# Performance work log

Hardware: AMD Instinct MI355X
Metric: run time of the kernel (lower is better)

## Reference

```python
import jax, jax.numpy as jnp
import numpy as np
import math

N = 100000   # nodes
E = 1600000  # edges (avg degree 16)
D = 128      # in_dim == out_dim
H = 8        # heads
DK = D // H  # 16


def setup_inputs() -> dict:
    key = jax.random.key(0)
    ks = jax.random.split(key, 16)
    s = 1.0 / math.sqrt(D)
    inp = {
        "h": jax.random.normal(ks[0], (N, D), dtype=jnp.float32),
        "src": jax.random.randint(ks[1], (E,), 0, N, dtype=jnp.int32),
        "dst": jax.random.randint(ks[2], (E,), 0, N, dtype=jnp.int32),
        # linear params (torch Linear: y = x @ W.T + b)
        "Wk": jax.random.normal(ks[3], (D, D), dtype=jnp.float32) * s,
        "bk": jnp.zeros((D,), dtype=jnp.float32),
        "Wq": jax.random.normal(ks[4], (D, D), dtype=jnp.float32) * s,
        "bq": jnp.zeros((D,), dtype=jnp.float32),
        "Wv": jax.random.normal(ks[5], (D, D), dtype=jnp.float32) * s,
        "bv": jnp.zeros((D,), dtype=jnp.float32),
        "Wa": jax.random.normal(ks[6], (D, D), dtype=jnp.float32) * s,
        "ba": jnp.zeros((D,), dtype=jnp.float32),
        # relation params
        "rel_att": jax.random.normal(ks[7], (H, DK, DK), dtype=jnp.float32) * (1.0 / math.sqrt(DK)),
        "rel_msg": jax.random.normal(ks[8], (H, DK, DK), dtype=jnp.float32) * (1.0 / math.sqrt(DK)),
        "rel_pri": jnp.ones((H,), dtype=jnp.float32),
        "skip": jnp.ones((1,), dtype=jnp.float32),
    }
    return inp


def reference(h, src, dst, Wk, bk, Wq, bq, Wv, bv, Wa, ba, rel_att, rel_msg, rel_pri, skip):
    sqrt_dk = math.sqrt(DK)
    # per-node projections -> [N, H, DK]
    k = (h @ Wk.T + bk).reshape(N, H, DK)
    q = (h @ Wq.T + bq).reshape(N, H, DK)
    v = (h @ Wv.T + bv).reshape(N, H, DK)
    # per-relation transforms on k and v
    k = jnp.einsum('nhd,hde->nhe', k, rel_att)
    v = jnp.einsum('nhd,hde->nhe', v, rel_msg)
    # edge scores: dot(q[dst], k[src]) per head -> [E, H]
    score = jnp.einsum('ehd,ehd->eh', q[dst], k[src])
    score = score * rel_pri / sqrt_dk
    # edge softmax normalized over incoming edges of each dst node
    smax = jax.ops.segment_max(score, dst, num_segments=N)        # [N, H]
    ex = jnp.exp(score - smax[dst])                               # [E, H]
    denom = jax.ops.segment_sum(ex, dst, num_segments=N)         # [N, H]
    attn = ex / denom[dst]                                       # [E, H]
    # weighted scatter-aggregation of source values
    msg = v[src] * attn[:, :, None]                               # [E, H, DK]
    t = jax.ops.segment_sum(msg, dst, num_segments=N)             # [N, H, DK]
    t = t.reshape(N, D)
    # target-specific aggregation with learned skip gate (dropout=0 eval, norm=Identity)
    trans_out = t @ Wa.T + ba
    alpha = jax.nn.sigmoid(skip[0])
    new_h = trans_out * alpha + h * (1.0 - alpha)
    return new_h
```

## Files before the change

### kernel.cpp

```cpp
#include <hip/hip_runtime.h>
#include <hip/hip_bf16.h>
#include <math.h>

#define NN 100000
#define EE 1600000
#define DD 128
#define HH 8
#define LDW 136
#define BSH 9
#define NB 196
#define EPB 8192
#define A_BLOCKS 196
#define GEMM_BLOCKS 782

typedef short short8 __attribute__((ext_vector_type(8)));
typedef float f32x4 __attribute__((ext_vector_type(4)));

__device__ __forceinline__ unsigned short f2bf(float f) {
    unsigned int u = __float_as_uint(f);
    u += 0x7fffu + ((u >> 16) & 1u);
    return (unsigned short)(u >> 16);
}
__device__ __forceinline__ float bf2f(unsigned short h) {
    return __uint_as_float((unsigned int)h << 16);
}
__device__ __forceinline__ void cvt8(const float4& a, const float4& b,
                                     short8& h8, short8& l8) {
    float vals[8] = {a.x, a.y, a.z, a.w, b.x, b.y, b.z, b.w};
    #pragma unroll
    for (int j = 0; j < 8; j++) {
        unsigned short hi = f2bf(vals[j]);
        h8[j] = (short)hi;
        l8[j] = (short)f2bf(vals[j] - bf2f(hi));
    }
}

__device__ __forceinline__ void prep_work(int which, int bx,
                             const float* __restrict__ Wq, const float* __restrict__ Wk,
                             const float* __restrict__ Wv, const float* __restrict__ Wa,
                             const float* __restrict__ bq, const float* __restrict__ bk,
                             const float* __restrict__ bv, const float* __restrict__ ba,
                             const float* __restrict__ rel_att, const float* __restrict__ rel_msg,
                             unsigned short* __restrict__ WH, unsigned short* __restrict__ WL,
                             float* __restrict__ BE) {
    int o = bx * 256 + threadIdx.x;
    int j = o >> 7, c = o & 127;
    float val;
    if (which == 0) {
        val = Wq[o];
        if (o < 128) BE[o] = bq[o];
    } else if (which == 3) {
        val = Wa[o];
        if (o < 128) BE[384 + o] = ba[o];
    } else {
        const float* rel = (which == 1) ? rel_att : rel_msg;
        const float* W   = (which == 1) ? Wk : Wv;
        const float* b   = (which == 1) ? bk : bv;
        int hh = j >> 4, e = j & 15;
        val = 0.f;
        #pragma unroll
        for (int d = 0; d < 16; d++)
            val += rel[hh * 256 + d * 16 + e] * W[(hh * 16 + d) * 128 + c];
        if (c == 0) {
            float bacc = 0.f;
            #pragma unroll
            for (int d = 0; d < 16; d++)
                bacc += b[hh * 16 + d] * rel[hh * 256 + d * 16 + e];
            BE[which * 128 + j] = bacc;
        }
    }
    unsigned short hi = f2bf(val);
    unsigned short lo = f2bf(val - bf2f(hi));
    WH[which * 16384 + o] = hi;
    WL[which * 16384 + o] = lo;
}

__global__ void prep_hist(const float* __restrict__ Wq, const float* __restrict__ Wk,
                          const float* __restrict__ Wv, const float* __restrict__ Wa,
                          const float* __restrict__ bq, const float* __restrict__ bk,
                          const float* __restrict__ bv, const float* __restrict__ ba,
                          const float* __restrict__ rel_att, const float* __restrict__ rel_msg,
                          unsigned short* __restrict__ WH, unsigned short* __restrict__ WL,
                          float* __restrict__ BE,
                          const int* __restrict__ dst, int* __restrict__ bcnt) {
    __shared__ int lh[NB];
    int bid = blockIdx.x;
    if (bid < 256) {
        prep_work(bid >> 6, bid & 63, Wq, Wk, Wv, Wa, bq, bk, bv, ba,
                  rel_att, rel_msg, WH, WL, BE);
    } else {
        int t = threadIdx.x;
        for (int i = t; i < NB; i += 256) lh[i] = 0;
        __syncthreads();
        int base = (bid - 256) * EPB;
        int cnt = min(EPB, EE - base);
        for (int i = t; i < cnt; i += 256)
            atomicAdd(&lh[dst[base + i] >> BSH], 1);
        __syncthreads();
        for (int i = t; i < NB; i += 256)
            if (lh[i]) atomicAdd(&bcnt[i], lh[i]);
    }
}

__device__ __forceinline__ void gemm_body(char* smemc, int base,
                         const float* __restrict__ x,
                         const unsigned short* __restrict__ WH,
                         const unsigned short* __restrict__ WL,
                         const float* __restrict__ BE, int nw,
                         float* __restrict__ out0, unsigned short* __restrict__ kvout,
                         const float* __restrict__ resid, const float* __restrict__ skip) {
    unsigned short* wh = (unsigned short*)smemc;
    unsigned short* wl = wh + 128 * LDW;
    int tid = threadIdx.x;
    int wv = tid >> 6, lane = tid & 63;
    int lrow = lane & 15, quad = lane >> 4;

    short8 ah[2][4], al[2][4];
    float4 fz = {0.f, 0.f, 0.f, 0.f};
    #pragma unroll
    for (int mt = 0; mt < 2; mt++) {
        int row = base + wv * 32 + mt * 16 + lrow;
        const float* xr = x + (size_t)row * 128;
        bool ok = (row < NN);
        #pragma unroll
        for (int kc = 0; kc < 4; kc++) {
            int off = kc * 32 + quad * 8;
            float4 a = ok ? *(const float4*)&xr[off] : fz;
            float4 b = ok ? *(const float4*)&xr[off + 4] : fz;
            cvt8(a, b, ah[mt][kc], al[mt][kc]);
        }
    }

    float alpha = 1.f, beta = 0.f;
    if (resid) {
        float sv = skip[0];
        alpha = 1.f / (1.f + expf(-sv));
        beta = 1.f - alpha;
    }

    for (int wi = 0; wi < nw; wi++) {
        __syncthreads();
        const unsigned short* WHp = WH + wi * 16384;
        const unsigned short* WLp = WL + wi * 16384;
        for (int i = tid; i < 128 * 16; i += 256) {
            int n = i >> 4, kq = (i & 15) << 3;
            *(uint4*)&wh[n * LDW + kq] = *(const uint4*)&WHp[n * 128 + kq];
            *(uint4*)&wl[n * LDW + kq] = *(const uint4*)&WLp[n * 128 + kq];
        }
        __syncthreads();

        f32x4 zero4 = {0.f, 0.f, 0.f, 0.f};
        f32x4 acc[2][8];
        #pragma unroll
        for (int a = 0; a < 2; a++)
            #pragma unroll
            for (int b = 0; b < 8; b++) acc[a][b] = zero4;

        #pragma unroll
        for (int kc = 0; kc < 4; kc++) {
            #pragma unroll
            for (int nt = 0; nt < 8; nt++) {
                int koff = kc * 32 + quad * 8;
                int brow = (nt * 16 + lrow) * LDW + koff;
                short8 bh = *(const short8*)&wh[brow];
                short8 bl = *(const short8*)&wl[brow];
                acc[0][nt] = __builtin_amdgcn_mfma_f32_16x16x32_bf16(ah[0][kc], bh, acc[0][nt], 0, 0, 0);
                acc[1][nt] = __builtin_amdgcn_mfma_f32_16x16x32_bf16(ah[1][kc], bh, acc[1][nt], 0, 0, 0);
                acc[0][nt] = __builtin_amdgcn_mfma_f32_16x16x32_bf16(al[0][kc], bh, acc[0][nt], 0, 0, 0);
                acc[1][nt] = __builtin_amdgcn_mfma_f32_16x16x32_bf16(al[1][kc], bh, acc[1][nt], 0, 0, 0);
                acc[0][nt] = __builtin_amdgcn_mfma_f32_16x16x32_bf16(ah[0][kc], bl, acc[0][nt], 0, 0, 0);
                acc[1][nt] = __builtin_amdgcn_mfma_f32_16x16x32_bf16(ah[1][kc], bl, acc[1][nt], 0, 0, 0);
            }
        }

        const float* be = BE + wi * 128;
        #pragma unroll
        for (int nt = 0; nt < 8; nt++) {
            int col = nt * 16 + lrow;
            float bb = be[col];
            #pragma unroll
            for (int mt = 0; mt < 2; mt++) {
                int r0 = base + wv * 32 + mt * 16 + quad * 4;
                #pragma unroll
                for (int rg = 0; rg < 4; rg++) {
                    int row = r0 + rg;
                    if (row < NN) {
                        float val = acc[mt][nt][rg] + bb;
                        if (wi == 0) {
                            if (resid) val = alpha * val + beta * resid[(size_t)row * 128 + col];
                            out0[(size_t)row * 128 + col] = val;
                        } else {
                            int pos = ((col >> 2) << 3) + ((wi - 1) << 2) + (col & 3);
                            kvout[(size_t)row * 256 + pos] = f2bf(val);
                        }
                    }
                }
            }
        }
    }
}

__launch_bounds__(256, 2)
__global__ void gemm_reg(const float* __restrict__ x,
                         const unsigned short* __restrict__ WH,
                         const unsigned short* __restrict__ WL,
                         const float* __restrict__ BE, int nw,
                         float* __restrict__ out0, unsigned short* __restrict__ kvout,
                         const float* __restrict__ resid, const float* __restrict__ skip) {
    __shared__ __align__(16) char smem[69632];
    gemm_body(smem, blockIdx.x * 128, x, WH, WL, BE, nw, out0, kvout, resid, skip);
}

__global__ void bucket_scan(const int* __restrict__ bcnt, int* __restrict__ btail,
                            int* __restrict__ sbase) {
    __shared__ int buf[2][256];
    int t = threadIdx.x;
    int v = (t < NB) ? bcnt[t] : 0;
    buf[0][t] = v;
    __syncthreads();
    int sb = 0;
    #pragma unroll
    for (int d = 1; d < 256; d <<= 1) {
        int x = buf[sb][t];
        if (t >= d) x += buf[sb][t - d];
        buf[sb ^ 1][t] = x;
        __syncthreads();
        sb ^= 1;
    }
    if (t < NB) {
        int excl = buf[sb][t] - v;
        btail[t] = excl;
        sbase[t] = excl;
    }
    if (t == 0) sbase[NB] = EE;
}

__device__ __forceinline__ void scatter_work(char* smemc, int bid,
                               const int* __restrict__ src, const int* __restrict__ dst,
                               int* __restrict__ btail, int* __restrict__ packed) {
    int2* staged = (int2*)smemc;
    int* hist   = (int*)(smemc + 65536);
    int* lstart = hist + NB;
    int* cursor = lstart + NB;
    int* gbase  = cursor + NB;
    int* sbuf   = gbase + NB;
    int t = threadIdx.x;
    for (int i = t; i < NB; i += 256) hist[i] = 0;
    __syncthreads();
    int base = bid * EPB;
    int cnt = min(EPB, EE - base);
    for (int i = t; i < cnt; i += 256)
        atomicAdd(&hist[dst[base + i] >> BSH], 1);
    __syncthreads();
    int v = (t < NB) ? hist[t] : 0;
    sbuf[t] = v;
    __syncthreads();
    int sb = 0;
    #pragma unroll
    for (int d = 1; d < 256; d <<= 1) {
        int x = sbuf[sb * 256 + t];
        if (t >= d) x += sbuf[sb * 256 + t - d];
        sbuf[(sb ^ 1) * 256 + t] = x;
        __syncthreads();
        sb ^= 1;
    }
    if (t < NB) {
        lstart[t] = sbuf[sb * 256 + t] - v;
        cursor[t] = sbuf[sb * 256 + t] - v;
    }
    __syncthreads();
    for (int i = t; i < cnt; i += 256) {
        int d = dst[base + i], s = src[base + i];
        int r = atomicAdd(&cursor[d >> BSH], 1);
        staged[r] = make_int2(s, d);
    }
    __syncthreads();
    for (int i = t; i < NB; i += 256) {
        int c = hist[i];
        if (c) gbase[i] = atomicAdd(&btail[i], c);
    }
    __syncthreads();
    for (int i = t; i < cnt; i += 256) {
        int2 e = staged[i];
        int b = e.y >> BSH;
        packed[gbase[b] + (i - lstart[b])] = ((e.y & 511) << 17) | e.x;
    }
}

__launch_bounds__(256, 1)
__global__ void bucket_scatter(const int* __restrict__ src, const int* __restrict__ dst,
                               int* __restrict__ btail, int* __restrict__ packed) {
    __shared__ __align__(16) char smem[70720];
    scatter_work(smem, blockIdx.x, src, dst, btail, packed);
}

__launch_bounds__(256, 2)
__global__ void gemm0_scatter(const float* __restrict__ x,
                              const unsigned short* __restrict__ WH,
                              const unsigned short* __restrict__ WL,
                              const float* __restrict__ BE,
                              float* __restrict__ q, unsigned short* __restrict__ kvout,
                              const int* __restrict__ src, const int* __restrict__ dst,
                              int* __restrict__ btail, int* __restrict__ packed) {
    __shared__ __align__(16) char smem[70720];
    if (blockIdx.x < A_BLOCKS)
        scatter_work(smem, blockIdx.x, src, dst, btail, packed);
    else
        gemm_body(smem, (blockIdx.x - A_BLOCKS) * 128, x, WH, WL, BE, 3,
                  q, kvout, nullptr, nullptr);
}

__launch_bounds__(512, 2)
__global__ void node_sort(const int* __restrict__ packed, const int* __restrict__ sbase,
                          int* __restrict__ offs, int* __restrict__ sorted_src) {
    __shared__ int hist[512], cursor[512];
    __shared__ int scn[2][512];
    int t = threadIdx.x;
    int b = blockIdx.x;
    int s0 = sbase[b], s1 = sbase[b + 1];
    hist[t] = 0;
    __syncthreads();
    for (int e = s0 + t; e < s1; e += 512)
        atomicAdd(&hist[packed[e] >> 17], 1);
    __syncthreads();
    int v = hist[t];
    scn[0][t] = v;
    __syncthreads();
    int sb = 0;
    #pragma unroll
    for (int d = 1; d < 512; d <<= 1) {
        int x = scn[sb][t];
        if (t >= d) x += scn[sb][t - d];
        scn[sb ^ 1][t] = x;
        __syncthreads();
        sb ^= 1;
    }
    int incl = scn[sb][t];
    int node = (b << BSH) + t;
    if (node < NN) offs[node] = s0 + incl;
    cursor[t] = s0 + incl - v;
    __syncthreads();
    for (int e = s0 + t; e < s1; e += 512) {
        int p = packed[e];
        int pos = atomicAdd(&cursor[p >> 17], 1);
        sorted_src[pos] = p & 0x1FFFF;
    }
}

__launch_bounds__(256, 4)
__global__ void fused_attn(const float* __restrict__ q,
                           const unsigned short* __restrict__ kv,
                           const int* __restrict__ offs, const int* __restrict__ sorted_src,
                           const float* __restrict__ rel_pri, float* __restrict__ t) {
    int wave = threadIdx.x >> 6, lane = threadIdx.x & 63;
    int n = blockIdx.x * 4 + wave;
    if (n >= NN) return;
    int half = lane >> 5;
    int sl = lane & 31;
    int hh = sl >> 2;
    int start = (n > 0) ? offs[n - 1] : 0;
    int cnt = offs[n] - start;

    float4 q4 = *(const float4*)&q[(size_t)n * 128 + sl * 4];
    float scale = rel_pri[hh] * 0.25f * 1.44269504088896340736f;
    q4.x *= scale; q4.y *= scale; q4.z *= scale; q4.w *= scale;

    const unsigned short* kvp = kv + sl * 8;

    float4 o4 = {0.f, 0.f, 0.f, 0.f};
    float denom = 0.f;

    int nIter = (cnt + 1) >> 1;
    #pragma unroll 4
    for (int it = 0; it < nIter; it++) {
        int j = 2 * it + half;
        float wgt = (j < cnt) ? 1.f : 0.f;
        int jj = (j < cnt) ? j : (cnt - 1);
        int s = sorted_src[start + jj];
        uint4 kvb = *(const uint4*)(kvp + (size_t)s * 256);
        float p = q4.x * bf2f((unsigned short)(kvb.x & 0xffff))
                + q4.y * bf2f((unsigned short)(kvb.x >> 16))
                + q4.z * bf2f((unsigned short)(kvb.y & 0xffff))
                + q4.w * bf2f((unsigned short)(kvb.y >> 16));
        p += __shfl_xor(p, 1);
        p += __shfl_xor(p, 2);
        float e = __builtin_amdgcn_exp2f(p) * wgt;
        denom += e;
        o4.x = fmaf(bf2f((unsigned short)(kvb.z & 0xffff)), e, o4.x);
        o4.y = fmaf(bf2f((unsigned short)(kvb.z >> 16)),    e, o4.y);
        o4.z = fmaf(bf2f((unsigned short)(kvb.w & 0xffff)), e, o4.z);
        o4.w = fmaf(bf2f((unsigned short)(kvb.w >> 16)),    e, o4.w);
    }

    denom += __shfl_xor(denom, 32);
    o4.x += __shfl_xor(o4.x, 32);
    o4.y += __shfl_xor(o4.y, 32);
    o4.z += __shfl_xor(o4.z, 32);
    o4.w += __shfl_xor(o4.w, 32);

    if (half == 0) {
        float inv = (cnt > 0) ? 1.f / denom : 0.f;
        o4.x *= inv; o4.y *= inv; o4.z *= inv; o4.w *= inv;
        *(float4*)&t[(size_t)n * 128 + sl * 4] = o4;
    }
}

extern "C" void kernel_launch(void* const* d_in, const int* in_sizes, int n_in,
                              void* d_out, int out_size, void* d_ws, size_t ws_size,
                              hipStream_t stream) {
    const float* h    = (const float*)d_in[0];
    const int*   src  = (const int*)d_in[1];
    const int*   dst  = (const int*)d_in[2];
    const float* Wk   = (const float*)d_in[3];
    const float* bk   = (const float*)d_in[4];
    const float* Wq   = (const float*)d_in[5];
    const float* bq   = (const float*)d_in[6];
    const float* Wv   = (const float*)d_in[7];
    const float* bv   = (const float*)d_in[8];
    const float* Wa   = (const float*)d_in[9];
    const float* ba   = (const float*)d_in[10];
    const float* rel_att = (const float*)d_in[11];
    const float* rel_msg = (const float*)d_in[12];
    const float* rel_pri = (const float*)d_in[13];
    const float* skip    = (const float*)d_in[14];
    float* out = (float*)d_out;

    unsigned short* kvbuf = (unsigned short*)d_ws;
    float* BE   = (float*)(kvbuf + (size_t)NN * 256);
    int* scratch = (int*)(BE + 512);
    int* bcnt  = scratch;
    int* btail = bcnt + NB;
    int* sbase = btail + NB;
    int* offs  = scratch + NN;
    int* bsum  = offs + NN;
    int* sorted_src = bsum + 128;
    unsigned short* WH = (unsigned short*)(sorted_src + EE);
    unsigned short* WL = WH + 4 * 16384;
    char* ws_end = (char*)(WL + 4 * 16384);
    size_t used = (size_t)(ws_end - (char*)d_ws);
    bool sep = (ws_size >= used + (size_t)EE * sizeof(int));
    int* packed = sep ? (int*)ws_end : (int*)kvbuf;
    float* q = out;
    float* t = out;

    hipMemsetAsync(bcnt, 0, NB * sizeof(int), stream);
    prep_hist<<<256 + A_BLOCKS, 256, 0, stream>>>(Wq, Wk, Wv, Wa, bq, bk, bv, ba,
                                                  rel_att, rel_msg, WH, WL, BE,
                                                  dst, bcnt);
    bucket_scan<<<1, 256, 0, stream>>>(bcnt, btail, sbase);

    if (sep) {
        gemm0_scatter<<<A_BLOCKS + GEMM_BLOCKS, 256, 0, stream>>>(
            h, WH, WL, BE, q, kvbuf, src, dst, btail, packed);
        node_sort<<<NB, 512, 0, stream>>>(packed, sbase, offs, sorted_src);
    } else {
        bucket_scatter<<<A_BLOCKS, 256, 0, stream>>>(src, dst, btail, packed);
        node_sort<<<NB, 512, 0, stream>>>(packed, sbase, offs, sorted_src);
        gemm_reg<<<GEMM_BLOCKS, 256, 0, stream>>>(h, WH, WL, BE, 3, q, kvbuf,
                                                  nullptr, nullptr);
    }

    fused_attn<<<(NN + 3) / 4, 256, 0, stream>>>(q, kvbuf, offs, sorted_src,
                                                 rel_pri, t);
    gemm_reg<<<GEMM_BLOCKS, 256, 0, stream>>>(t, WH + 3 * 16384, WL + 3 * 16384,
                                              BE + 384, 1, out, nullptr,
                                              h, skip);
}
```

Before: 481.9 us.

## Split projection GEMM across scatter and sort launches; process two edges per half-wave

The first projection GEMM's row blocks are split: 316 blocks run alongside the bucket scatter, and the rest run in a new combined kernel alongside the per-bucket node sort. The node sort is rewritten for 256 threads so it can share a launch with GEMM blocks, with each thread handling two histogram bins in the scan. The attention loop now processes two edges per half-wave per iteration, issuing both KV gathers before the math. The aim is to hide the standalone sort behind GEMM work and to get more memory-level parallelism in the gather, at the cost of more registers and an uneven split of work between the two launches.

```diff
diff --git a/kernel.cpp b/kernel.cpp
--- a/kernel.cpp
+++ b/kernel.cpp
@@ -12,6 +12,7 @@
 #define EPB 8192
 #define A_BLOCKS 196
 #define GEMM_BLOCKS 782
+#define G1 316
 
 typedef short short8 __attribute__((ext_vector_type(8)));
 typedef float f32x4 __attribute__((ext_vector_type(4)));
@@ -287,11 +288,60 @@
     }
 }
 
+__device__ __forceinline__ void sort_work(char* smemc, int b,
+                          const int* __restrict__ packed, const int* __restrict__ sbase,
+                          int* __restrict__ offs, int* __restrict__ sorted_src) {
+    int* hist   = (int*)smemc;
+    int* cursor = hist + 512;
+    int* scn    = cursor + 512;
+    int t = threadIdx.x;
+    int s0 = sbase[b], s1 = sbase[b + 1];
+    hist[t] = 0; hist[t + 256] = 0;
+    __syncthreads();
+    for (int e = s0 + t; e < s1; e += 256)
+        atomicAdd(&hist[packed[e] >> 17], 1);
+    __syncthreads();
+    int a  = hist[2 * t];
+    int bb = hist[2 * t + 1];
+    scn[t] = a + bb;
+    __syncthreads();
+    int sb = 0;
+    #pragma unroll
+    for (int d = 1; d < 256; d <<= 1) {
+        int x = scn[sb * 256 + t];
+        if (t >= d) x += scn[sb * 256 + t - d];
+        scn[(sb ^ 1) * 256 + t] = x;
+        __syncthreads();
+        sb ^= 1;
+    }
+    int inclPair = scn[sb * 256 + t];
+    int incl1 = inclPair;
+    int incl0 = inclPair - bb;
+    int node0 = (b << BSH) + 2 * t;
+    if (node0 < NN)     offs[node0]     = s0 + incl0;
+    if (node0 + 1 < NN) offs[node0 + 1] = s0 + incl1;
+    cursor[2 * t]     = s0 + incl0 - a;
+    cursor[2 * t + 1] = s0 + incl1 - bb;
+    __syncthreads();
+    for (int e = s0 + t; e < s1; e += 256) {
+        int p = packed[e];
+        int pos = atomicAdd(&cursor[p >> 17], 1);
+        sorted_src[pos] = p & 0x1FFFF;
+    }
+}
+
 __launch_bounds__(256, 1)
 __global__ void bucket_scatter(const int* __restrict__ src, const int* __restrict__ dst,
                                int* __restrict__ btail, int* __restrict__ packed) {
     __shared__ __align__(16) char smem[70720];
     scatter_work(smem, blockIdx.x, src, dst, btail, packed);
+}
+
+__launch_bounds__(256, 2)
+__global__ void node_sort_k(const int* __restrict__ packed, const int* __restrict__ sbase,
+                            int* __restrict__ offs, int* __restrict__ sorted_src) {
+    __shared__ __align__(16) char smem[6144];
+    sort_work(smem, blockIdx.x, packed, sbase, offs, sorted_src);
 }
 
 __launch_bounds__(256, 2)
@@ -310,41 +360,20 @@
                   q, kvout, nullptr, nullptr);
 }
 
-__launch_bounds__(512, 2)
-__global__ void node_sort(const int* __restrict__ packed, const int* __restrict__ sbase,
-                          int* __restrict__ offs, int* __restrict__ sorted_src) {
-    __shared__ int hist[512], cursor[512];
-    __shared__ int scn[2][512];
-    int t = threadIdx.x;
-    int b = blockIdx.x;
-    int s0 = sbase[b], s1 = sbase[b + 1];
-    hist[t] = 0;
-    __syncthreads();
-    for (int e = s0 + t; e < s1; e += 512)
-        atomicAdd(&hist[packed[e] >> 17], 1);
-    __syncthreads();
-    int v = hist[t];
-    scn[0][t] = v;
-    __syncthreads();
-    int sb = 0;
-    #pragma unroll
-    for (int d = 1; d < 512; d <<= 1) {
-        int x = scn[sb][t];
-        if (t >= d) x += scn[sb][t - d];
-        scn[sb ^ 1][t] = x;
-        __syncthreads();
-        sb ^= 1;
-    }
-    int incl = scn[sb][t];
-    int node = (b << BSH) + t;
-    if (node < NN) offs[node] = s0 + incl;
-    cursor[t] = s0 + incl - v;
-    __syncthreads();
-    for (int e = s0 + t; e < s1; e += 512) {
-        int p = packed[e];
-        int pos = atomicAdd(&cursor[p >> 17], 1);
-        sorted_src[pos] = p & 0x1FFFF;
-    }
+__launch_bounds__(256, 2)
+__global__ void gemm0_sort(const float* __restrict__ x,
+                           const unsigned short* __restrict__ WH,
+                           const unsigned short* __restrict__ WL,
+                           const float* __restrict__ BE,
+                           float* __restrict__ q, unsigned short* __restrict__ kvout,
+                           const int* __restrict__ packed, const int* __restrict__ sbase,
+                           int* __restrict__ offs, int* __restrict__ sorted_src) {
+    __shared__ __align__(16) char smem[70720];
+    if (blockIdx.x < NB)
+        sort_work(smem, blockIdx.x, packed, sbase, offs, sorted_src);
+    else
+        gemm_body(smem, (G1 + blockIdx.x - NB) * 128, x, WH, WL, BE, 3,
+                  q, kvout, nullptr, nullptr);
 }
 
 __launch_bounds__(256, 4)
@@ -366,30 +395,48 @@
     q4.x *= scale; q4.y *= scale; q4.z *= scale; q4.w *= scale;
 
     const unsigned short* kvp = kv + sl * 8;
+    const int* ss = sorted_src + start;
 
     float4 o4 = {0.f, 0.f, 0.f, 0.f};
     float denom = 0.f;
 
-    int nIter = (cnt + 1) >> 1;
-    #pragma unroll 4
+    int nIter = (cnt + 3) >> 2;
+    #pragma unroll 2
     for (int it = 0; it < nIter; it++) {
-        int j = 2 * it + half;
-        float wgt = (j < cnt) ? 1.f : 0.f;
-        int jj = (j < cnt) ? j : (cnt - 1);
-        int s = sorted_src[start + jj];
-        uint4 kvb = *(const uint4*)(kvp + (size_t)s * 256);
-        float p = q4.x * bf2f((unsigned short)(kvb.x & 0xffff))
-                + q4.y * bf2f((unsigned short)(kvb.x >> 16))
-                + q4.z * bf2f((unsigned short)(kvb.y & 0xffff))
-                + q4.w * bf2f((unsigned short)(kvb.y >> 16));
-        p += __shfl_xor(p, 1);
-        p += __shfl_xor(p, 2);
-        float e = __builtin_amdgcn_exp2f(p) * wgt;
-        denom += e;
-        o4.x = fmaf(bf2f((unsigned short)(kvb.z & 0xffff)), e, o4.x);
-        o4.y = fmaf(bf2f((unsigned short)(kvb.z >> 16)),    e, o4.y);
-        o4.z = fmaf(bf2f((unsigned short)(kvb.w & 0xffff)), e, o4.z);
-        o4.w = fmaf(bf2f((unsigned short)(kvb.w >> 16)),    e, o4.w);
+        int j0 = 4 * it + 2 * half;
+        int j1 = j0 + 1;
+        float w0 = (j0 < cnt) ? 1.f : 0.f;
+        float w1 = (j1 < cnt) ? 1.f : 0.f;
+        int jj0 = (j0 < cnt) ? j0 : (cnt - 1);
+        int jj1 = (j1 < cnt) ? j1 : (cnt - 1);
+        int s0 = ss[jj0];
+        int s1 = ss[jj1];
+        uint4 ka = *(const uint4*)(kvp + (size_t)s0 * 256);
+        uint4 kb = *(const uint4*)(kvp + (size_t)s1 * 256);
+
+        float pa = q4.x * bf2f((unsigned short)(ka.x & 0xffff))
+                 + q4.y * bf2f((unsigned short)(ka.x >> 16))
+                 + q4.z * bf2f((unsigned short)(ka.y & 0xffff))
+                 + q4.w * bf2f((unsigned short)(ka.y >> 16));
+        float pb = q4.x * bf2f((unsigned short)(kb.x & 0xffff))
+                 + q4.y * bf2f((unsigned short)(kb.x >> 16))
+                 + q4.z * bf2f((unsigned short)(kb.y & 0xffff))
+                 + q4.w * bf2f((unsigned short)(kb.y >> 16));
+        pa += __shfl_xor(pa, 1);
+        pa += __shfl_xor(pa, 2);
+        pb += __shfl_xor(pb, 1);
+        pb += __shfl_xor(pb, 2);
+        float ea = __builtin_amdgcn_exp2f(pa) * w0;
+        float eb = __builtin_amdgcn_exp2f(pb) * w1;
+        denom += ea + eb;
+        o4.x = fmaf(bf2f((unsigned short)(ka.z & 0xffff)), ea, o4.x);
+        o4.y = fmaf(bf2f((unsigned short)(ka.z >> 16)),    ea, o4.y);
+        o4.z = fmaf(bf2f((unsigned short)(ka.w & 0xffff)), ea, o4.z);
+        o4.w = fmaf(bf2f((unsigned short)(ka.w >> 16)),    ea, o4.w);
+        o4.x = fmaf(bf2f((unsigned short)(kb.z & 0xffff)), eb, o4.x);
+        o4.y = fmaf(bf2f((unsigned short)(kb.z >> 16)),    eb, o4.y);
+        o4.z = fmaf(bf2f((unsigned short)(kb.w & 0xffff)), eb, o4.z);
+        o4.w = fmaf(bf2f((unsigned short)(kb.w >> 16)),    eb, o4.w);
     }
 
     denom += __shfl_xor(denom, 32);
@@ -450,12 +497,13 @@
     bucket_scan<<<1, 256, 0, stream>>>(bcnt, btail, sbase);
 
     if (sep) {
-        gemm0_scatter<<<A_BLOCKS + GEMM_BLOCKS, 256, 0, stream>>>(
+        gemm0_scatter<<<A_BLOCKS + G1, 256, 0, stream>>>(
             h, WH, WL, BE, q, kvbuf, src, dst, btail, packed);
-        node_sort<<<NB, 512, 0, stream>>>(packed, sbase, offs, sorted_src);
+        gemm0_sort<<<NB + (GEMM_BLOCKS - G1), 256, 0, stream>>>(
+            h, WH, WL, BE, q, kvbuf, packed, sbase, offs, sorted_src);
     } else {
         bucket_scatter<<<A_BLOCKS, 256, 0, stream>>>(src, dst, btail, packed);
-        node_sort<<<NB, 512, 0, stream>>>(packed, sbase, offs, sorted_src);
+        node_sort_k<<<NB, 256, 0, stream>>>(packed, sbase, offs, sorted_src);
         gemm_reg<<<GEMM_BLOCKS, 256, 0, stream>>>(h, WH, WL, BE, 3, q, kvbuf,
                                                   nullptr, nullptr);
     }
```

New measurement: 477.3 us (median of 2 runs). About the same (-0.9%).
